# Kernel optimization log

Hardware: AMD Instinct MI355X
Metric: run time of the kernel (lower is better)

Reference implementation:

```python
import jax, jax.numpy as jnp
import numpy as np

NEG_BIG = -9.0e15  # matches -9000000000000000.0 fill in the torch code


def setup_inputs() -> dict:
    key = jax.random.key(0)
    ks = jax.random.split(key, 8)
    N, Fin, Fout = 8192, 256, 128
    input = jax.random.normal(ks[0], (N, Fin), dtype=jnp.float32)
    adj = jax.random.randint(ks[1], (N, N), 0, 2, dtype=jnp.int32)
    s_fc = 1.0 / np.sqrt(Fin)
    s_at = 1.0 / np.sqrt(Fout)
    W_fc = jax.random.normal(ks[2], (Fin, Fout), dtype=jnp.float32) * s_fc
    b_fc = jax.random.normal(ks[3], (Fout,), dtype=jnp.float32) * s_fc
    w_ax = jax.random.normal(ks[4], (Fout, 1), dtype=jnp.float32) * s_at
    b_ax = jax.random.normal(ks[5], (1,), dtype=jnp.float32) * s_at
    w_an = jax.random.normal(ks[6], (Fout, 1), dtype=jnp.float32) * s_at
    b_an = jax.random.normal(ks[7], (1,), dtype=jnp.float32) * s_at
    return {"input": input, "adj": adj, "W_fc": W_fc, "b_fc": b_fc,
            "w_ax": w_ax, "b_ax": b_ax, "w_an": w_an, "b_an": b_an}


def reference(input, adj, W_fc, b_fc, w_ax, b_ax, w_an, b_an):
    # x = fc(input): [N, Fout]
    x = input @ W_fc + b_fc
    # rank-1 additive scores: att_x(x) [N,1] + att_nei(x).T [1,N] -> [N,N]
    x_att = x @ w_ax + b_ax          # [N, 1]
    neib_att = (x @ w_an + b_an).T   # [1, N]
    ws = x_att + neib_att            # [N, N]
    # adjacency mask + row softmax
    ws = jnp.where(adj > 0, ws, NEG_BIG)
    ws = jax.nn.softmax(ws, axis=1)
    # dense aggregation + residual + ELU (dropout is identity in eval)
    out = jax.nn.elu(x + ws @ x)
    return out
```

## Files before the change

### kernel.cpp

```cpp
#include <hip/hip_runtime.h>
#include <hip/hip_bf16.h>
#include <math.h>


using f32x4  = __attribute__((ext_vector_type(4))) float;
using bf16x8 = __attribute__((ext_vector_type(8))) short;

#define N_NODES 8192
#define FIN     256
#define FOUT    128
#define NPAD    144
#define NSPLIT  8
#define KCHUNK  (N_NODES / NSPLIT)

#define X_OFF    0u
#define T_OFF    (X_OFF + N_NODES*FOUT*4u)
#define PMAX_OFF (T_OFF + N_NODES*4u)
#define GMAX_OFF (PMAX_OFF + 1024u)
#define YT_OFF   (GMAX_OFF + 512u)
#define P_OFF    (YT_OFF + (size_t)NPAD*N_NODES*2u)
#define ADJP_OFF (P_OFF + (size_t)NSPLIT*N_NODES*NPAD*4u)

__device__ __forceinline__ unsigned short f2bf(float f) {
  unsigned int u = __float_as_uint(f);
  unsigned int r = (u + 0x7FFFu + ((u >> 16) & 1u)) >> 16;
  return (unsigned short)r;
}

__global__ __launch_bounds__(256) void k0_pack(const int* __restrict__ adj,
    unsigned long long* __restrict__ adjP) {
  const int lane = threadIdx.x & 63, w = threadIdx.x >> 6;
  const int row = blockIdx.x * 4 + w;
  const int* src = adj + (size_t)row * N_NODES;
  unsigned long long mine = 0;
  for (int h = 0; h < 2; ++h) {
    #pragma unroll 16
    for (int g = 0; g < 64; ++g) {
      int v = src[h * 4096 + g * 64 + lane];
      unsigned long long m = __ballot(v != 0);
      if (lane == g) mine = m;
    }
    adjP[(size_t)row * 128 + h * 64 + lane] = mine;
  }
}

__global__ __launch_bounds__(256) void k1_fc(const float* __restrict__ in,
    const float* __restrict__ Wfc, const float* __restrict__ bfc,
    float* __restrict__ x) {
  __shared__ float sm[16 * FIN];
  const int tid = threadIdx.x;
  const int r0  = blockIdx.x * 16;
  const float4* gin = reinterpret_cast<const float4*>(in + (size_t)r0 * FIN);
  float4* sm4 = reinterpret_cast<float4*>(sm);
  #pragma unroll
  for (int i = 0; i < 4; i++) sm4[i * 256 + tid] = gin[i * 256 + tid];
  __syncthreads();
  const int d = tid & 127, g = tid >> 7;
  const float bias = bfc[d];
  float acc[8];
  #pragma unroll
  for (int r = 0; r < 8; r++) acc[r] = bias;
  const float4* s4 = reinterpret_cast<const float4*>(sm);
  for (int k = 0; k < FIN; k += 4) {
    float w0 = Wfc[(k + 0) * FOUT + d];
    float w1 = Wfc[(k + 1) * FOUT + d];
    float w2 = Wfc[(k + 2) * FOUT + d];
    float w3 = Wfc[(k + 3) * FOUT + d];
    #pragma unroll
    for (int r = 0; r < 8; r++) {
      float4 iv = s4[((g * 8 + r) * FIN + k) >> 2];
      acc[r] = fmaf(iv.x, w0, acc[r]);
      acc[r] = fmaf(iv.y, w1, acc[r]);
      acc[r] = fmaf(iv.z, w2, acc[r]);
      acc[r] = fmaf(iv.w, w3, acc[r]);
    }
  }
  #pragma unroll
  for (int r = 0; r < 8; r++)
    x[(size_t)(r0 + g * 8 + r) * FOUT + d] = acc[r];
}

__global__ __launch_bounds__(256) void k2_att(const float* __restrict__ x,
    const float* __restrict__ wan, const float* __restrict__ ban,
    float* __restrict__ t, float* __restrict__ pmax) {
  __shared__ float wm[4];
  const int tid = threadIdx.x, lane = tid & 63, w = tid >> 6;
  const float w0 = wan[lane], w1 = wan[lane + 64];
  const float bb = ban[0];
  float tmax = -1e30f;
  const int rbase = blockIdx.x * 32 + w * 8;
  for (int rr = 0; rr < 8; rr++) {
    const int row = rbase + rr;
    float p = x[(size_t)row * FOUT + lane] * w0
            + x[(size_t)row * FOUT + 64 + lane] * w1;
    #pragma unroll
    for (int m = 1; m < 64; m <<= 1) p += __shfl_xor(p, m);
    const float tv = p + bb;
    if (lane == 0) t[row] = tv;
    tmax = fmaxf(tmax, tv);
  }
  if (lane == 0) wm[w] = tmax;
  __syncthreads();
  if (tid == 0)
    pmax[blockIdx.x] = fmaxf(fmaxf(wm[0], wm[1]), fmaxf(wm[2], wm[3]));
}

__global__ void k3_gmax(const float* __restrict__ pmax, float* __restrict__ gmax) {
  float v = fmaxf(fmaxf(pmax[threadIdx.x], pmax[threadIdx.x + 64]),
                  fmaxf(pmax[threadIdx.x + 128], pmax[threadIdx.x + 192]));
  #pragma unroll
  for (int m = 1; m < 64; m <<= 1) v = fmaxf(v, __shfl_xor(v, m));
  if (threadIdx.x == 0) gmax[0] = v;
}

__global__ __launch_bounds__(256) void k4_y(const float* __restrict__ x,
    const float* __restrict__ t, const float* __restrict__ gmax,
    unsigned short* __restrict__ Yf) {
  __shared__ unsigned short sm[NPAD * 64];
  const int tid = threadIdx.x, lane = tid & 63, w = tid >> 6;
  const int jj = lane, j = blockIdx.x * 64 + jj;
  const float e = expf(t[j] - gmax[0]);
  const float4* x4 = reinterpret_cast<const float4*>(x + (size_t)j * FOUT + w * 32);
  #pragma unroll
  for (int dd = 0; dd < 8; dd++) {
    float4 xv = x4[dd];
    const int c = w * 32 + dd * 4;
    sm[(c + 0) * 64 + jj] = f2bf(e * xv.x);
    sm[(c + 1) * 64 + jj] = f2bf(e * xv.y);
    sm[(c + 2) * 64 + jj] = f2bf(e * xv.z);
    sm[(c + 3) * 64 + jj] = f2bf(e * xv.w);
  }
  #pragma unroll
  for (int i = 0; i < 4; i++) {
    const int c = 128 + w * 4 + i;
    sm[c * 64 + jj] = (c == 128) ? f2bf(e) : (unsigned short)0;
  }
  __syncthreads();
  for (int c5 = w; c5 < 18; c5 += 4) {
    const int wnd = c5 / 9, nf = c5 % 9;
    const int srcIdx = (nf * 16 + (lane & 15)) * 64 + wnd * 32 + (lane >> 4) * 8;
    bf16x8 v = *reinterpret_cast<const bf16x8*>(&sm[srcIdx]);
    const size_t Wg = (size_t)blockIdx.x * 2 + wnd;
    *reinterpret_cast<bf16x8*>(Yf + (Wg * 9 + nf) * 512 + lane * 8) = v;
  }
}

__global__ __launch_bounds__(256) void k5_gemm(
    const unsigned long long* __restrict__ adjP,
    const unsigned short* __restrict__ Yf, float* __restrict__ P) {
  const int tid  = threadIdx.x;
  const int lane = tid & 63, w = tid >> 6;
  const int bm = blockIdx.x, s = blockIdx.y;
  const int q  = lane >> 4, r = lane & 15;
  const int row_g = bm * 64 + w * 16 + r;
  const unsigned long long* ap = adjP + (size_t)row_g * 128 + s * 16;
  const unsigned short* bbase = Yf + (size_t)s * 32 * 9 * 512 + lane * 8;
  const int qs = q * 8;

  f32x4 acc[9];
  #pragma unroll
  for (int nf = 0; nf < 9; nf++) acc[nf] = (f32x4){0.f, 0.f, 0.f, 0.f};

#define LOAD_B(dst_, wnd_) { \
    const unsigned short* p_ = bbase + (size_t)(wnd_) * 9 * 512; \
    _Pragma("unroll") \
    for (int nf = 0; nf < 9; nf++) \
      dst_[nf] = *reinterpret_cast<const bf16x8*>(p_ + nf * 512); \
  }

#define MFMA_BITS(b_, B_) { \
    union { bf16x8 v; unsigned int u[4]; } af; \
    _Pragma("unroll") \
    for (int i2 = 0; i2 < 4; i2++) { \
      const unsigned bq = (b_) >> (2 * i2); \
      af.u[i2] = ((bq & 1u) ? 0x3F80u : 0u) | ((bq & 2u) ? 0x3F800000u : 0u); \
    } \
    _Pragma("unroll") \
    for (int nf = 0; nf < 9; nf++) \
      acc[nf] = __builtin_amdgcn_mfma_f32_16x16x32_bf16(af.v, B_[nf], acc[nf], 0, 0, 0); \
  }

  bf16x8 Be[9], Bo[9];
  unsigned long long Ac = ap[0];
  unsigned long long An = ap[1];
  LOAD_B(Be, 0);
  LOAD_B(Bo, 1);

  for (int t = 0; t < 16; ++t) {
    const unsigned lo = (unsigned)Ac, hi = (unsigned)(Ac >> 32);
    const unsigned be_ = (lo >> qs) & 0xFFu;
    MFMA_BITS(be_, Be);
    if (t < 15) LOAD_B(Be, 2 * t + 2);
    const unsigned bo_ = (hi >> qs) & 0xFFu;
    MFMA_BITS(bo_, Bo);
    if (t < 15) LOAD_B(Bo, 2 * t + 3);
    Ac = An;
    if (t < 14) An = ap[t + 2];
  }
#undef LOAD_B
#undef MFMA_BITS

  float* Pp = P + (size_t)s * N_NODES * NPAD;
  const int colb = lane & 15;
  #pragma unroll
  for (int nf = 0; nf < 9; nf++) {
    if (nf == 8 && colb != 0) continue;
    #pragma unroll
    for (int rr = 0; rr < 4; rr++) {
      const int grow = bm * 64 + w * 16 + q * 4 + rr;
      Pp[(size_t)grow * NPAD + nf * 16 + colb] = acc[nf][rr];
    }
  }
}

__global__ __launch_bounds__(256) void k6_fin(const float* __restrict__ P,
    const float* __restrict__ x, float* __restrict__ out) {
  const int gid = blockIdx.x * 256 + threadIdx.x;
  const int i = gid >> 7, d = gid & 127;
  const size_t base = (size_t)i * NPAD;
  float num = 0.f, Z = 0.f;
  #pragma unroll
  for (int s = 0; s < NSPLIT; s++) {
    num += P[(size_t)s * N_NODES * NPAD + base + d];
    Z   += P[(size_t)s * N_NODES * NPAD + base + 128];
  }
  const float agg = (Z > 0.f) ? num / Z : 0.f;
  const float v = x[(size_t)i * FOUT + d] + agg;
  out[gid] = (v > 0.f) ? v : expm1f(v);
}

extern "C" void kernel_launch(void* const* d_in, const int* in_sizes, int n_in,
                              void* d_out, int out_size, void* d_ws, size_t ws_size,
                              hipStream_t stream) {
  const float* input = (const float*)d_in[0];
  const int*   adj   = (const int*)d_in[1];
  const float* Wfc   = (const float*)d_in[2];
  const float* bfc   = (const float*)d_in[3];
  const float* wan   = (const float*)d_in[6];
  const float* ban   = (const float*)d_in[7];

  char* ws = (char*)d_ws;
  float*              x    = (float*)(ws + X_OFF);
  float*              t    = (float*)(ws + T_OFF);
  float*              pmax = (float*)(ws + PMAX_OFF);
  float*              gmax = (float*)(ws + GMAX_OFF);
  unsigned short*     Yf   = (unsigned short*)(ws + YT_OFF);
  float*              P    = (float*)(ws + P_OFF);
  unsigned long long* adjP = (unsigned long long*)(ws + ADJP_OFF);
  float*              out  = (float*)d_out;

  k0_pack<<<dim3(2048),        dim3(256), 0, stream>>>(adj, adjP);
  k1_fc  <<<dim3(512),         dim3(256), 0, stream>>>(input, Wfc, bfc, x);
  k2_att <<<dim3(256),         dim3(256), 0, stream>>>(x, wan, ban, t, pmax);
  k3_gmax<<<dim3(1),           dim3(64),  0, stream>>>(pmax, gmax);
  k4_y   <<<dim3(128),         dim3(256), 0, stream>>>(x, t, gmax, Yf);
  k5_gemm<<<dim3(128, NSPLIT), dim3(256), 0, stream>>>(adjP, Yf, P);
  k6_fin <<<dim3(4096),        dim3(256), 0, stream>>>(P, x, out);
}
```

Baseline: 454.9 us.

## Fuse attention score and global max into FC kernel; widen GEMM blocks

Computes the per-row neighbor attention score inside the FC kernel from register accumulators. The global max is now reduced with an atomicMax on an order-preserving unsigned key, which removes two kernel launches and a re-read of x. The GEMM kernel now uses 512-thread blocks covering 128 rows. Its explicit double-buffered B prefetch is replaced by plain per-window loads, which reduces register pressure to allow more occupancy but leaves latency hiding to the compiler and scheduler. The atomic key is zeroed in the adjacency pack kernel, which adds an ordering dependency on stream serialization.

```diff
diff --git a/kernel.cpp b/kernel.cpp
--- a/kernel.cpp
+++ b/kernel.cpp
@@ -15,9 +15,8 @@
 
 #define X_OFF    0u
 #define T_OFF    (X_OFF + N_NODES*FOUT*4u)
-#define PMAX_OFF (T_OFF + N_NODES*4u)
-#define GMAX_OFF (PMAX_OFF + 1024u)
-#define YT_OFF   (GMAX_OFF + 512u)
+#define GKEY_OFF (T_OFF + N_NODES*4u)
+#define YT_OFF   (GKEY_OFF + 512u)
 #define P_OFF    (YT_OFF + (size_t)NPAD*N_NODES*2u)
 #define ADJP_OFF (P_OFF + (size_t)NSPLIT*N_NODES*NPAD*4u)
 
@@ -27,8 +26,17 @@
   return (unsigned short)r;
 }
 
+__device__ __forceinline__ unsigned fkey(float f) {
+  unsigned b = __float_as_uint(f);
+  return (b & 0x80000000u) ? ~b : (b | 0x80000000u);
+}
+__device__ __forceinline__ float fkey_dec(unsigned k) {
+  return __uint_as_float((k & 0x80000000u) ? (k & 0x7FFFFFFFu) : ~k);
+}
+
 __global__ __launch_bounds__(256) void k0_pack(const int* __restrict__ adj,
-    unsigned long long* __restrict__ adjP) {
+    unsigned long long* __restrict__ adjP, unsigned* __restrict__ gkey) {
+  if (blockIdx.x == 0 && threadIdx.x == 0) gkey[0] = 0u;
   const int lane = threadIdx.x & 63, w = threadIdx.x >> 6;
   const int row = blockIdx.x * 4 + w;
   const int* src = adj + (size_t)row * N_NODES;
@@ -46,8 +54,11 @@
 
 __global__ __launch_bounds__(256) void k1_fc(const float* __restrict__ in,
     const float* __restrict__ Wfc, const float* __restrict__ bfc,
-    float* __restrict__ x) {
+    const float* __restrict__ wan, const float* __restrict__ ban,
+    float* __restrict__ x, float* __restrict__ t, unsigned* __restrict__ gkey) {
   __shared__ float sm[16 * FIN];
+  __shared__ float part[2][16];
+  __shared__ float tval[16];
   const int tid = threadIdx.x;
   const int r0  = blockIdx.x * 16;
   const float4* gin = reinterpret_cast<const float4*>(in + (size_t)r0 * FIN);
@@ -78,48 +89,39 @@
   #pragma unroll
   for (int r = 0; r < 8; r++)
     x[(size_t)(r0 + g * 8 + r) * FOUT + d] = acc[r];
-}
-
-__global__ __launch_bounds__(256) void k2_att(const float* __restrict__ x,
-    const float* __restrict__ wan, const float* __restrict__ ban,
-    float* __restrict__ t, float* __restrict__ pmax) {
-  __shared__ float wm[4];
-  const int tid = threadIdx.x, lane = tid & 63, w = tid >> 6;
-  const float w0 = wan[lane], w1 = wan[lane + 64];
-  const float bb = ban[0];
-  float tmax = -1e30f;
-  const int rbase = blockIdx.x * 32 + w * 8;
-  for (int rr = 0; rr < 8; rr++) {
-    const int row = rbase + rr;
-    float p = x[(size_t)row * FOUT + lane] * w0
-            + x[(size_t)row * FOUT + 64 + lane] * w1;
+
+  const float wv = wan[d];
+  const int lane = tid & 63, half = (tid >> 6) & 1;
+  #pragma unroll
+  for (int r = 0; r < 8; r++) {
+    float p = acc[r] * wv;
     #pragma unroll
     for (int m = 1; m < 64; m <<= 1) p += __shfl_xor(p, m);
-    const float tv = p + bb;
-    if (lane == 0) t[row] = tv;
-    tmax = fmaxf(tmax, tv);
-  }
-  if (lane == 0) wm[w] = tmax;
-  __syncthreads();
-  if (tid == 0)
-    pmax[blockIdx.x] = fmaxf(fmaxf(wm[0], wm[1]), fmaxf(wm[2], wm[3]));
-}
-
-__global__ void k3_gmax(const float* __restrict__ pmax, float* __restrict__ gmax) {
-  float v = fmaxf(fmaxf(pmax[threadIdx.x], pmax[threadIdx.x + 64]),
-                  fmaxf(pmax[threadIdx.x + 128], pmax[threadIdx.x + 192]));
-  #pragma unroll
-  for (int m = 1; m < 64; m <<= 1) v = fmaxf(v, __shfl_xor(v, m));
-  if (threadIdx.x == 0) gmax[0] = v;
+    if (lane == 0) part[half][g * 8 + r] = p;
+  }
+  __syncthreads();
+  if (tid < 16) {
+    const float tv = part[0][tid] + part[1][tid] + ban[0];
+    t[r0 + tid] = tv;
+    tval[tid] = tv;
+  }
+  __syncthreads();
+  if (tid == 0) {
+    float m = tval[0];
+    #pragma unroll
+    for (int i = 1; i < 16; i++) m = fmaxf(m, tval[i]);
+    atomicMax(gkey, fkey(m));
+  }
 }
 
 __global__ __launch_bounds__(256) void k4_y(const float* __restrict__ x,
-    const float* __restrict__ t, const float* __restrict__ gmax,
+    const float* __restrict__ t, const unsigned* __restrict__ gkey,
     unsigned short* __restrict__ Yf) {
   __shared__ unsigned short sm[NPAD * 64];
   const int tid = threadIdx.x, lane = tid & 63, w = tid >> 6;
   const int jj = lane, j = blockIdx.x * 64 + jj;
-  const float e = expf(t[j] - gmax[0]);
+  const float gm = fkey_dec(gkey[0]);
+  const float e = expf(t[j] - gm);
   const float4* x4 = reinterpret_cast<const float4*>(x + (size_t)j * FOUT + w * 32);
   #pragma unroll
   for (int dd = 0; dd < 8; dd++) {
@@ -145,14 +147,14 @@
   }
 }
 
-__global__ __launch_bounds__(256) void k5_gemm(
+__global__ __launch_bounds__(512, 4) void k5_gemm(
     const unsigned long long* __restrict__ adjP,
     const unsigned short* __restrict__ Yf, float* __restrict__ P) {
   const int tid  = threadIdx.x;
   const int lane = tid & 63, w = tid >> 6;
   const int bm = blockIdx.x, s = blockIdx.y;
   const int q  = lane >> 4, r = lane & 15;
-  const int row_g = bm * 64 + w * 16 + r;
+  const int row_g = bm * 128 + w * 16 + r;
   const unsigned long long* ap = adjP + (size_t)row_g * 128 + s * 16;
   const unsigned short* bbase = Yf + (size_t)s * 32 * 9 * 512 + lane * 8;
   const int qs = q * 8;
@@ -161,14 +163,12 @@
   #pragma unroll
   for (int nf = 0; nf < 9; nf++) acc[nf] = (f32x4){0.f, 0.f, 0.f, 0.f};
 
-#define LOAD_B(dst_, wnd_) { \
-    const unsigned short* p_ = bbase + (size_t)(wnd_) * 9 * 512; \
+#define MFMA_WIN(b_, woff_) { \
+    bf16x8 bv[9]; \
+    const unsigned short* p_ = bbase + (size_t)(woff_) * (9 * 512); \
     _Pragma("unroll") \
     for (int nf = 0; nf < 9; nf++) \
-      dst_[nf] = *reinterpret_cast<const bf16x8*>(p_ + nf * 512); \
-  }
-
-#define MFMA_BITS(b_, B_) { \
+      bv[nf] = *reinterpret_cast<const bf16x8*>(p_ + nf * 512); \
     union { bf16x8 v; unsigned int u[4]; } af; \
     _Pragma("unroll") \
     for (int i2 = 0; i2 < 4; i2++) { \
@@ -177,28 +177,19 @@
     } \
     _Pragma("unroll") \
     for (int nf = 0; nf < 9; nf++) \
-      acc[nf] = __builtin_amdgcn_mfma_f32_16x16x32_bf16(af.v, B_[nf], acc[nf], 0, 0, 0); \
-  }
-
-  bf16x8 Be[9], Bo[9];
+      acc[nf] = __builtin_amdgcn_mfma_f32_16x16x32_bf16(af.v, bv[nf], acc[nf], 0, 0, 0); \
+  }
+
   unsigned long long Ac = ap[0];
   unsigned long long An = ap[1];
-  LOAD_B(Be, 0);
-  LOAD_B(Bo, 1);
-
   for (int t = 0; t < 16; ++t) {
     const unsigned lo = (unsigned)Ac, hi = (unsigned)(Ac >> 32);
-    const unsigned be_ = (lo >> qs) & 0xFFu;
-    MFMA_BITS(be_, Be);
-    if (t < 15) LOAD_B(Be, 2 * t + 2);
-    const unsigned bo_ = (hi >> qs) & 0xFFu;
-    MFMA_BITS(bo_, Bo);
-    if (t < 15) LOAD_B(Bo, 2 * t + 3);
+    MFMA_WIN(((lo >> qs) & 0xFFu), 2 * t);
+    MFMA_WIN(((hi >> qs) & 0xFFu), 2 * t + 1);
     Ac = An;
     if (t < 14) An = ap[t + 2];
   }
-#undef LOAD_B
-#undef MFMA_BITS
+#undef MFMA_WIN
 
   float* Pp = P + (size_t)s * N_NODES * NPAD;
   const int colb = lane & 15;
@@ -207,7 +198,7 @@
     if (nf == 8 && colb != 0) continue;
     #pragma unroll
     for (int rr = 0; rr < 4; rr++) {
-      const int grow = bm * 64 + w * 16 + q * 4 + rr;
+      const int grow = bm * 128 + w * 16 + q * 4 + rr;
       Pp[(size_t)grow * NPAD + nf * 16 + colb] = acc[nf][rr];
     }
   }
@@ -242,18 +233,16 @@
   char* ws = (char*)d_ws;
   float*              x    = (float*)(ws + X_OFF);
   float*              t    = (float*)(ws + T_OFF);
-  float*              pmax = (float*)(ws + PMAX_OFF);
-  float*              gmax = (float*)(ws + GMAX_OFF);
+  unsigned*           gkey = (unsigned*)(ws + GKEY_OFF);
   unsigned short*     Yf   = (unsigned short*)(ws + YT_OFF);
   float*              P    = (float*)(ws + P_OFF);
   unsigned long long* adjP = (unsigned long long*)(ws + ADJP_OFF);
   float*              out  = (float*)d_out;
 
-  k0_pack<<<dim3(2048),        dim3(256), 0, stream>>>(adj, adjP);
-  k1_fc  <<<dim3(512),         dim3(256), 0, stream>>>(input, Wfc, bfc, x);
-  k2_att <<<dim3(256),         dim3(256), 0, stream>>>(x, wan, ban, t, pmax);
-  k3_gmax<<<dim3(1),           dim3(64),  0, stream>>>(pmax, gmax);
-  k4_y   <<<dim3(128),         dim3(256), 0, stream>>>(x, t, gmax, Yf);
-  k5_gemm<<<dim3(128, NSPLIT), dim3(256), 0, stream>>>(adjP, Yf, P);
-  k6_fin <<<dim3(4096),        dim3(256), 0, stream>>>(P, x, out);
-}
+  k0_pack<<<dim3(2048),       dim3(256), 0, stream>>>(adj, adjP, gkey);
+  k1_fc  <<<dim3(512),        dim3(256), 0, stream>>>(input, Wfc, bfc, wan, ban,
+                                                      x, t, gkey);
+  k4_y   <<<dim3(128),        dim3(256), 0, stream>>>(x, t, gkey, Yf);
+  k5_gemm<<<dim3(64, NSPLIT), dim3(512), 0, stream>>>(adjP, Yf, P);
+  k6_fin <<<dim3(4096),       dim3(256), 0, stream>>>(P, x, out);
+}
```

Measured after the change: 459.0 us. No clear change (+0.9%).
